# Kernel tuning notes

Measured on AMD Instinct MI355X. Metric: run time of the kernel, lower is better.

## Reference

```python
import jax, jax.numpy as jnp
import numpy as np

NQ = 10000   # num_q
N = 512      # n (seq len)
D = 512      # d (model dim)
H = 8        # attention heads
LW = 64      # local window
B = 16       # batch


def _mha(q, k, v, wi, bi, wo, bo, nh, mask=None):
    # torch nn.MultiheadAttention math (eval mode, dropout off), batch-first inputs
    Bq, S, d = q.shape
    hd = d // nh
    wq, wk, wv = jnp.split(wi, 3, axis=0)
    bq, bk, bv = jnp.split(bi, 3)

    def proj(x, w, b):
        y = x @ w.T + b
        return y.reshape(x.shape[0], x.shape[1], nh, hd).transpose(0, 2, 1, 3)  # [B,h,S,hd]

    Q = proj(q, wq, bq)
    K = proj(k, wk, bk)
    V = proj(v, wv, bv)
    s = jnp.einsum('bhqe,bhke->bhqk', Q, K) / jnp.sqrt(jnp.asarray(hd, q.dtype))
    if mask is not None:
        s = jnp.where(mask[None, None], -jnp.inf, s)
    w = jax.nn.softmax(s, axis=-1)
    o = jnp.einsum('bhqk,bhke->bhqe', w, V).transpose(0, 2, 1, 3).reshape(Bq, S, d)
    return o @ wo.T + bo, w.mean(axis=1)  # avg over heads like torch default


def _ln(x, g, b):
    m = x.mean(-1, keepdims=True)
    v = ((x - m) ** 2).mean(-1, keepdims=True)
    return (x - m) / jnp.sqrt(v + 1e-5) * g + b


def setup_inputs() -> dict:
    key = jax.random.key(0)
    ks = iter(jax.random.split(key, 40))
    f = lambda *sh: jax.random.normal(next(ks), sh, jnp.float32) * 0.02
    inp = {
        'q': jax.random.randint(next(ks), (B, N), 0, NQ, jnp.int32),
        'r': jax.random.randint(next(ks), (B, N), 0, 2, jnp.int32),
        'qry': jax.random.randint(next(ks), (B, N), 0, NQ, jnp.int32),
        'M_emb': f(2 * NQ, D),
        'E_emb': f(NQ, D),
        'P': f(N, D),
    }
    for nm in ['base', 'local', 'glob', 'cross']:
        inp[nm + '_in_w'] = f(3 * D, D)
        inp[nm + '_in_b'] = jnp.zeros((3 * D,), jnp.float32)
        inp[nm + '_out_w'] = f(D, D)
        inp[nm + '_out_b'] = jnp.zeros((D,), jnp.float32)
    inp['ln1_g'] = jnp.ones((D,), jnp.float32)
    inp['ln1_b'] = jnp.zeros((D,), jnp.float32)
    inp['w1'] = f(D, D)
    inp['b1'] = jnp.zeros((D,), jnp.float32)
    inp['w2'] = f(D, D)
    inp['b2'] = jnp.zeros((D,), jnp.float32)
    inp['ln2_g'] = jnp.ones((D,), jnp.float32)
    inp['ln2_b'] = jnp.zeros((D,), jnp.float32)
    inp['pred_w'] = f(1, D)
    inp['pred_b'] = jnp.zeros((1,), jnp.float32)
    return inp


def reference(q, r, qry, M_emb, E_emb, P,
              base_in_w, base_in_b, base_out_w, base_out_b,
              local_in_w, local_in_b, local_out_w, local_out_b,
              glob_in_w, glob_in_b, glob_out_w, glob_out_b,
              cross_in_w, cross_in_b, cross_out_w, cross_out_b,
              ln1_g, ln1_b, w1, b1, w2, b2, ln2_g, ln2_b, pred_w, pred_b):
    x = q + NQ * r
    M = M_emb[x] + P[None]          # [B,N,D], positional added as in torch code
    E = E_emb[qry]                  # [B,N,D]
    cm = jnp.triu(jnp.ones((N, N), bool), 1)

    S_base, attn_w = _mha(E, M, M, base_in_w, base_in_b, base_out_w, base_out_b, H, cm)
    S_base = _ln(S_base + M + E, ln1_g, ln1_b)

    lm = jnp.triu(jnp.ones((LW, LW), bool), 1)
    s_loc_in = S_base[:, -LW:, :]
    S_loc, _ = _mha(s_loc_in, s_loc_in, s_loc_in, local_in_w, local_in_b, local_out_w, local_out_b, H, lm)
    S_local = jnp.concatenate([jnp.zeros((S_base.shape[0], N - LW, D), S_base.dtype), S_loc], axis=1)

    S_global, _ = _mha(S_base, S_base, S_base, glob_in_w, glob_in_b, glob_out_w, glob_out_b, H, cm)
    S_cross, _ = _mha(S_base, S_local, S_local, cross_in_w, cross_in_b, cross_out_w, cross_out_b, H, None)

    S = S_base + S_local + S_global + S_cross
    F = jax.nn.relu(S @ w1.T + b1) @ w2.T + b2
    F = _ln(F + S, ln2_g, ln2_b)
    p = jax.nn.sigmoid(F @ pred_w.T + pred_b)[..., 0]   # [B,N]
    return p, attn_w
```

## Files before the change

### kernel.cpp

```cpp
#include <hip/hip_runtime.h>
#include <hip/hip_bf16.h>

#define D_MODEL 512
#define NHEAD 8
#define NSEQ 512
#define BATCH 16
#define LWIN 64

typedef short s16x8 __attribute__((ext_vector_type(8)));
typedef float f32x4 __attribute__((ext_vector_type(4)));

__device__ inline unsigned short f2bf(float f) {
    unsigned int u = __float_as_uint(f);
    u = (u + 0x7fffu + ((u >> 16) & 1u)) >> 16;
    return (unsigned short)u;
}

struct WP { const float* p[10]; };
__global__ __launch_bounds__(256) void wconv_kernel(WP wp, unsigned short* __restrict__ Wb)
{
    const long e = ((long)blockIdx.x * 256 + threadIdx.x) * 4;
    const float* src; long loc;
    if (e < 3145728) { int rg = (int)(e / 786432); src = wp.p[rg]; loc = e - (long)rg * 786432; }
    else { long j = e - 3145728; int rg = (int)(j >> 18); src = wp.p[4 + rg]; loc = j - ((long)rg << 18); }
    float4 v = *(const float4*)(src + loc);
    ushort4 o; o.x = f2bf(v.x); o.y = f2bf(v.y); o.z = f2bf(v.z); o.w = f2bf(v.w);
    *(ushort4*)(Wb + e) = o;
}

__global__ __launch_bounds__(128) void embed_kernel(
    const int* __restrict__ q, const int* __restrict__ r, const int* __restrict__ qry,
    const float* __restrict__ M_emb, const float* __restrict__ E_emb,
    const float* __restrict__ P, float* __restrict__ Mf, float* __restrict__ Ef,
    unsigned short* __restrict__ Mb, unsigned short* __restrict__ Eb)
{
    const int t = blockIdx.x;
    const int n = t & (NSEQ - 1);
    const int x = q[t] + 10000 * r[t];
    const int e = qry[t];
    const int i = threadIdx.x;
    float4 a = ((const float4*)(M_emb + (long)x * D_MODEL))[i];
    float4 p4 = ((const float4*)(P + (long)n * D_MODEL))[i];
    float4 ev = ((const float4*)(E_emb + (long)e * D_MODEL))[i];
    float4 mv = make_float4(a.x + p4.x, a.y + p4.y, a.z + p4.z, a.w + p4.w);
    ((float4*)(Mf + (long)t * D_MODEL))[i] = mv;
    ((float4*)(Ef + (long)t * D_MODEL))[i] = ev;
    ushort4 mb; mb.x = f2bf(mv.x); mb.y = f2bf(mv.y); mb.z = f2bf(mv.z); mb.w = f2bf(mv.w);
    ushort4 eb; eb.x = f2bf(ev.x); eb.y = f2bf(ev.y); eb.z = f2bf(ev.z); eb.w = f2bf(ev.w);
    *(ushort4*)(Mb + (long)t * D_MODEL + i * 4) = mb;
    *(ushort4*)(Eb + (long)t * D_MODEL + i * 4) = eb;
}

__global__ __launch_bounds__(256) void gemm_bf16(
    const unsigned short* __restrict__ A, const unsigned short* __restrict__ W,
    const float* __restrict__ bias, unsigned short* __restrict__ Cb,
    float* __restrict__ Cf, int ldc, int relu)
{
    __shared__ unsigned short As[128 * 40];
    __shared__ unsigned short Ws[128 * 40];
    const int tid = threadIdx.x, lane = tid & 63, wid = tid >> 6;
    const int m0 = blockIdx.y * 128, n0 = blockIdx.x * 128;
    const int mbase = (wid >> 1) * 64, nbase = (wid & 1) * 64;
    const int srow = tid >> 2, scol = (tid & 3) * 8;
    const unsigned short* Ap = A + (long)(m0 + srow) * 512 + scol;
    const unsigned short* Wp = W + (long)(n0 + srow) * 512 + scol;
    const int fr = lane & 15;
    const int fk = (lane >> 4) * 8;

    f32x4 acc[4][4];
    #pragma unroll
    for (int i = 0; i < 4; ++i)
        #pragma unroll
        for (int j = 0; j < 4; ++j) acc[i][j] = (f32x4){0.f, 0.f, 0.f, 0.f};

    for (int k0 = 0; k0 < 512; k0 += 32) {
        s16x8 a0 = *(const s16x8*)(Ap + k0);
        s16x8 a1 = *(const s16x8*)(Ap + 64 * 512 + k0);
        s16x8 w0 = *(const s16x8*)(Wp + k0);
        s16x8 w1 = *(const s16x8*)(Wp + 64 * 512 + k0);
        __syncthreads();
        *(s16x8*)&As[srow * 40 + scol] = a0;
        *(s16x8*)&As[(64 + srow) * 40 + scol] = a1;
        *(s16x8*)&Ws[srow * 40 + scol] = w0;
        *(s16x8*)&Ws[(64 + srow) * 40 + scol] = w1;
        __syncthreads();
        s16x8 af[4], wf[4];
        #pragma unroll
        for (int t = 0; t < 4; ++t) {
            af[t] = *(const s16x8*)&As[(mbase + t * 16 + fr) * 40 + fk];
            wf[t] = *(const s16x8*)&Ws[(nbase + t * 16 + fr) * 40 + fk];
        }
        #pragma unroll
        for (int i = 0; i < 4; ++i)
            #pragma unroll
            for (int j = 0; j < 4; ++j)
                acc[i][j] = __builtin_amdgcn_mfma_f32_16x16x32_bf16(af[i], wf[j], acc[i][j], 0, 0, 0);
    }

    const int q4 = (lane >> 4) * 4;
    #pragma unroll
    for (int j = 0; j < 4; ++j) {
        const int col = n0 + nbase + j * 16 + fr;
        const float bv = bias[col];
        #pragma unroll
        for (int i = 0; i < 4; ++i) {
            const int row = m0 + mbase + i * 16 + q4;
            #pragma unroll
            for (int rg = 0; rg < 4; ++rg) {
                float v = acc[i][j][rg] + bv;
                if (relu) v = fmaxf(v, 0.f);
                const long off = (long)(row + rg) * ldc + col;
                if (Cb) Cb[off] = f2bf(v);
                if (Cf) Cf[off] = v;
            }
        }
    }
}

__global__ __launch_bounds__(256) void flash_mfma(
    const unsigned short* __restrict__ Q, const unsigned short* __restrict__ K,
    const unsigned short* __restrict__ V, unsigned short* __restrict__ O,
    float* __restrict__ stats, int Nq, int Nkv, int ldq, int ldkv, int causal)
{
    __shared__ __align__(16) unsigned short Ks[64 * 72];
    __shared__ __align__(16) unsigned short Pl[64 * 72];
    __shared__ __align__(16) unsigned int   Vt[64 * 36];

    const int tid = threadIdx.x, lane = tid & 63, w = tid >> 6;
    const int lm = lane & 15, lq = lane >> 4;
    const int qt = blockIdx.x, h = blockIdx.y, b = blockIdx.z;

    s16x8 aq0, aq1;
    {
        const unsigned short* qp = Q + ((long)b * Nq + qt * 64 + w * 16 + lm) * ldq + h * 64 + lq * 8;
        aq0 = *(const s16x8*)qp;
        aq1 = *(const s16x8*)(qp + 32);
    }

    float m_r[4] = {-INFINITY, -INFINITY, -INFINITY, -INFINITY};
    float l_r[4] = {0.f, 0.f, 0.f, 0.f};
    f32x4 o_acc[4];
    #pragma unroll
    for (int t = 0; t < 4; ++t) o_acc[t] = (f32x4){0.f, 0.f, 0.f, 0.f};

    const int nkt = causal ? (qt + 1) : (Nkv >> 6);

    for (int kt = 0; kt < nkt; ++kt) {
        __syncthreads();
        {
            const long kb = ((long)b * Nkv + kt * 64) * ldkv + h * 64;
            #pragma unroll
            for (int c = 0; c < 2; ++c) {
                const int ch = c * 256 + tid;
                const int key = ch >> 3, d = (ch & 7) * 8;
                s16x8 kv = *(const s16x8*)(K + kb + (long)key * ldkv + d);
                *(s16x8*)&Ks[key * 72 + d] = kv;
            }
        }
        {
            const int kp = tid >> 3, dc = (tid & 7) * 8;
            const unsigned short* vp = V + ((long)b * Nkv + kt * 64 + 2 * kp) * ldkv + h * 64 + dc;
            uint4 va = *(const uint4*)vp;
            uint4 vb = *(const uint4*)(vp + ldkv);
            unsigned pw[8];
            pw[0] = (va.x & 0xffffu) | (vb.x << 16);
            pw[1] = (va.x >> 16)     | (vb.x & 0xffff0000u);
            pw[2] = (va.y & 0xffffu) | (vb.y << 16);
            pw[3] = (va.y >> 16)     | (vb.y & 0xffff0000u);
            pw[4] = (va.z & 0xffffu) | (vb.z << 16);
            pw[5] = (va.z >> 16)     | (vb.z & 0xffff0000u);
            pw[6] = (va.w & 0xffffu) | (vb.w << 16);
            pw[7] = (va.w >> 16)     | (vb.w & 0xffff0000u);
            #pragma unroll
            for (int j = 0; j < 8; ++j) {
                const int row = dc + j;
                const int col = ((((kp >> 2) ^ (row >> 3)) & 7) << 2) | (kp & 3);
                Vt[row * 36 + col] = pw[j];
            }
        }
        __syncthreads();

        f32x4 sc[4];
        #pragma unroll
        for (int t = 0; t < 4; ++t) sc[t] = (f32x4){0.f, 0.f, 0.f, 0.f};
        #pragma unroll
        for (int t = 0; t < 4; ++t) {
            s16x8 bk0 = *(const s16x8*)&Ks[(t * 16 + lm) * 72 + lq * 8];
            s16x8 bk1 = *(const s16x8*)&Ks[(t * 16 + lm) * 72 + lq * 8 + 32];
            sc[t] = __builtin_amdgcn_mfma_f32_16x16x32_bf16(aq0, bk0, sc[t], 0, 0, 0);
            sc[t] = __builtin_amdgcn_mfma_f32_16x16x32_bf16(aq1, bk1, sc[t], 0, 0, 0);
        }
        #pragma unroll
        for (int t = 0; t < 4; ++t)
            #pragma unroll
            for (int r = 0; r < 4; ++r) sc[t][r] *= 0.125f;

        if (causal && kt == qt) {
            #pragma unroll
            for (int t = 0; t < 4; ++t)
                #pragma unroll
                for (int r = 0; r < 4; ++r)
                    if (t * 16 + lm > w * 16 + lq * 4 + r) sc[t][r] = -INFINITY;
        }

        #pragma unroll
        for (int r = 0; r < 4; ++r) {
            float mt = fmaxf(fmaxf(sc[0][r], sc[1][r]), fmaxf(sc[2][r], sc[3][r]));
            #pragma unroll
            for (int off = 1; off < 16; off <<= 1) mt = fmaxf(mt, __shfl_xor(mt, off));
            const float mn = fmaxf(m_r[r], mt);
            const float al = __expf(m_r[r] - mn);
            m_r[r] = mn;
            float rs = 0.f;
            #pragma unroll
            for (int t = 0; t < 4; ++t) {
                float p = __expf(sc[t][r] - mn);
                sc[t][r] = p; rs += p;
                o_acc[t][r] *= al;
                Pl[(w * 16 + lq * 4 + r) * 72 + t * 16 + lm] = f2bf(p);
            }
            #pragma unroll
            for (int off = 1; off < 16; off <<= 1) rs += __shfl_xor(rs, off);
            l_r[r] = l_r[r] * al + rs;
        }

        #pragma unroll
        for (int ks = 0; ks < 2; ++ks) {
            s16x8 ap = *(const s16x8*)&Pl[(w * 16 + lm) * 72 + lq * 8 + ks * 32];
            #pragma unroll
            for (int t = 0; t < 4; ++t) {
                const int row = t * 16 + lm;
                const int gs = ((lq + 4 * ks) ^ (row >> 3)) & 7;
                s16x8 bv = *(const s16x8*)&Vt[row * 36 + gs * 4];
                o_acc[t] = __builtin_amdgcn_mfma_f32_16x16x32_bf16(ap, bv, o_acc[t], 0, 0, 0);
            }
        }
    }

    float inv[4];
    #pragma unroll
    for (int r = 0; r < 4; ++r) inv[r] = 1.0f / l_r[r];
    #pragma unroll
    for (int t = 0; t < 4; ++t)
        #pragma unroll
        for (int r = 0; r < 4; ++r)
            O[((long)b * Nq + qt * 64 + w * 16 + lq * 4 + r) * D_MODEL + h * 64 + t * 16 + lm]
                = f2bf(o_acc[t][r] * inv[r]);
    if (stats && lm == 0) {
        #pragma unroll
        for (int r = 0; r < 4; ++r) {
            const long row = qt * 64 + w * 16 + lq * 4 + r;
            const long idx = (((long)b * NHEAD + h) * Nq + row) * 2;
            stats[idx] = m_r[r]; stats[idx + 1] = l_r[r];
        }
    }
}

__global__ __launch_bounds__(256) void attn_w_kernel(
    const unsigned short* __restrict__ Q, const unsigned short* __restrict__ K,
    const float* __restrict__ stats, float* __restrict__ AW, int ldq, int ldk)
{
    const int kt = blockIdx.x, qt = blockIdx.y, b = blockIdx.z;
    const int tid = threadIdx.x;
    if (kt > qt) {
        const int tx = tid & 15, ty = tid >> 4;
        #pragma unroll
        for (int i = 0; i < 4; ++i)
            *(float4*)(AW + ((long)b * NSEQ + qt * 64 + ty * 4 + i) * NSEQ + kt * 64 + tx * 4)
                = make_float4(0.f, 0.f, 0.f, 0.f);
        return;
    }
    __shared__ __align__(16) unsigned short Ks[64 * 72];
    const int lane = tid & 63, w = tid >> 6;
    const int lm = lane & 15, lq = lane >> 4;

    f32x4 aw[4];
    #pragma unroll
    for (int t = 0; t < 4; ++t) aw[t] = (f32x4){0.f, 0.f, 0.f, 0.f};

    for (int h = 0; h < NHEAD; ++h) {
        __syncthreads();
        {
            const long kb = ((long)b * NSEQ + kt * 64) * ldk + h * 64;
            #pragma unroll
            for (int c = 0; c < 2; ++c) {
                const int ch = c * 256 + tid;
                const int key = ch >> 3, d = (ch & 7) * 8;
                s16x8 kv = *(const s16x8*)(K + kb + (long)key * ldk + d);
                *(s16x8*)&Ks[key * 72 + d] = kv;
            }
        }
        __syncthreads();
        s16x8 aq0, aq1;
        {
            const unsigned short* qp = Q + ((long)b * NSEQ + qt * 64 + w * 16 + lm) * ldq + h * 64 + lq * 8;
            aq0 = *(const s16x8*)qp;
            aq1 = *(const s16x8*)(qp + 32);
        }
        f32x4 sc[4];
        #pragma unroll
        for (int t = 0; t < 4; ++t) sc[t] = (f32x4){0.f, 0.f, 0.f, 0.f};
        #pragma unroll
        for (int t = 0; t < 4; ++t) {
            s16x8 bk0 = *(const s16x8*)&Ks[(t * 16 + lm) * 72 + lq * 8];
            s16x8 bk1 = *(const s16x8*)&Ks[(t * 16 + lm) * 72 + lq * 8 + 32];
            sc[t] = __builtin_amdgcn_mfma_f32_16x16x32_bf16(aq0, bk0, sc[t], 0, 0, 0);
            sc[t] = __builtin_amdgcn_mfma_f32_16x16x32_bf16(aq1, bk1, sc[t], 0, 0, 0);
        }
        #pragma unroll
        for (int r = 0; r < 4; ++r) {
            float2 ml = *(const float2*)(stats +
                (((long)b * NHEAD + h) * NSEQ + qt * 64 + w * 16 + lq * 4 + r) * 2);
            const float sub = ml.x, sca = 0.125f / ml.y;
            #pragma unroll
            for (int t = 0; t < 4; ++t) {
                const bool masked = (kt == qt) && (t * 16 + lm > w * 16 + lq * 4 + r);
                if (!masked) aw[t][r] += __expf(sc[t][r] * 0.125f - sub) * sca;
            }
        }
    }
    #pragma unroll
    for (int t = 0; t < 4; ++t)
        #pragma unroll
        for (int r = 0; r < 4; ++r)
            AW[((long)b * NSEQ + qt * 64 + w * 16 + lq * 4 + r) * NSEQ + kt * 64 + t * 16 + lm]
                = aw[t][r];
}

__global__ __launch_bounds__(256) void ln_kernel(
    const float* __restrict__ X, const float* __restrict__ R1,
    const float* __restrict__ R2, const float* __restrict__ g,
    const float* __restrict__ bb, float* __restrict__ outf,
    unsigned short* __restrict__ outb)
{
    const long row = blockIdx.x;
    const int tid = threadIdx.x;
    __shared__ float red[256];
    const long base = row * D_MODEL;
    float v0 = X[base + tid], v1 = X[base + tid + 256];
    if (R1) { v0 += R1[base + tid]; v1 += R1[base + tid + 256]; }
    if (R2) { v0 += R2[base + tid]; v1 += R2[base + tid + 256]; }
    red[tid] = v0 + v1; __syncthreads();
    for (int s = 128; s > 0; s >>= 1) {
        if (tid < s) red[tid] += red[tid + s];
        __syncthreads();
    }
    const float mean = red[0] * (1.f / 512.f);
    __syncthreads();
    const float d0 = v0 - mean, d1 = v1 - mean;
    red[tid] = d0 * d0 + d1 * d1; __syncthreads();
    for (int s = 128; s > 0; s >>= 1) {
        if (tid < s) red[tid] += red[tid + s];
        __syncthreads();
    }
    const float rstd = rsqrtf(red[0] * (1.f / 512.f) + 1e-5f);
    const float y0 = d0 * rstd * g[tid] + bb[tid];
    const float y1 = d1 * rstd * g[tid + 256] + bb[tid + 256];
    if (outf) { outf[base + tid] = y0; outf[base + tid + 256] = y1; }
    if (outb) { outb[base + tid] = f2bf(y0); outb[base + tid + 256] = f2bf(y1); }
}

__global__ __launch_bounds__(128) void extract_last64(
    const unsigned short* __restrict__ Sb, unsigned short* __restrict__ out)
{
    const int t = blockIdx.x;
    const int b = t >> 6, j = t & 63;
    const uint2* src = (const uint2*)(Sb + ((long)b * NSEQ + (NSEQ - LWIN) + j) * D_MODEL);
    uint2* dst = (uint2*)(out + (long)t * D_MODEL);
    dst[threadIdx.x] = src[threadIdx.x];
}

__global__ __launch_bounds__(128) void build_slocal(
    const float* __restrict__ Tloc, float* __restrict__ Sf, unsigned short* __restrict__ Sb)
{
    const int t = blockIdx.x;
    const int b = t >> 9, n = t & 511;
    const int i = threadIdx.x;
    float4 v;
    if (n < NSEQ - LWIN) v = make_float4(0.f, 0.f, 0.f, 0.f);
    else v = ((const float4*)(Tloc + ((long)b * LWIN + (n - (NSEQ - LWIN))) * D_MODEL))[i];
    ((float4*)(Sf + (long)t * D_MODEL))[i] = v;
    ushort4 u; u.x = f2bf(v.x); u.y = f2bf(v.y); u.z = f2bf(v.z); u.w = f2bf(v.w);
    *(ushort4*)(Sb + (long)t * D_MODEL + i * 4) = u;
}

__global__ __launch_bounds__(256) void sum4_kernel(
    const float* __restrict__ a, const float* __restrict__ b,
    const float* __restrict__ c, const float* __restrict__ d,
    float* __restrict__ of, unsigned short* __restrict__ ob, int n4)
{
    const int i = blockIdx.x * blockDim.x + threadIdx.x;
    if (i < n4) {
        float4 x = ((const float4*)a)[i];
        float4 y = ((const float4*)b)[i];
        float4 z = ((const float4*)c)[i];
        float4 w = ((const float4*)d)[i];
        float4 s = make_float4(x.x + y.x + z.x + w.x, x.y + y.y + z.y + w.y,
                               x.z + y.z + z.z + w.z, x.w + y.w + z.w + w.w);
        ((float4*)of)[i] = s;
        ushort4 u; u.x = f2bf(s.x); u.y = f2bf(s.y); u.z = f2bf(s.z); u.w = f2bf(s.w);
        *(ushort4*)(ob + (long)i * 4) = u;
    }
}

__global__ __launch_bounds__(256) void pred_kernel(
    const float* __restrict__ F, const float* __restrict__ pw,
    const float* __restrict__ pb, float* __restrict__ out)
{
    const int w = threadIdx.x >> 6, lane = threadIdx.x & 63;
    const long row = (long)blockIdx.x * 4 + w;
    const float* fr = F + row * D_MODEL;
    float s = 0.f;
    #pragma unroll
    for (int i = 0; i < 8; ++i) s += fr[lane + i * 64] * pw[lane + i * 64];
    #pragma unroll
    for (int off = 32; off > 0; off >>= 1) s += __shfl_down(s, off);
    if (lane == 0) out[row] = 1.f / (1.f + __expf(-(s + pb[0])));
}

extern "C" void kernel_launch(void* const* d_in, const int* in_sizes, int n_in,
                              void* d_out, int out_size, void* d_ws, size_t ws_size,
                              hipStream_t stream)
{
    const int*   q          = (const int*)d_in[0];
    const int*   r          = (const int*)d_in[1];
    const int*   qry        = (const int*)d_in[2];
    const float* M_emb      = (const float*)d_in[3];
    const float* E_emb      = (const float*)d_in[4];
    const float* P          = (const float*)d_in[5];
    const float* base_in_w  = (const float*)d_in[6];
    const float* base_in_b  = (const float*)d_in[7];
    const float* base_out_w = (const float*)d_in[8];
    const float* base_out_b = (const float*)d_in[9];
    const float* local_in_w = (const float*)d_in[10];
    const float* local_in_b = (const float*)d_in[11];
    const float* local_out_w= (const float*)d_in[12];
    const float* local_out_b= (const float*)d_in[13];
    const float* glob_in_w  = (const float*)d_in[14];
    const float* glob_in_b  = (const float*)d_in[15];
    const float* glob_out_w = (const float*)d_in[16];
    const float* glob_out_b = (const float*)d_in[17];
    const float* cross_in_w = (const float*)d_in[18];
    const float* cross_in_b = (const float*)d_in[19];
    const float* cross_out_w= (const float*)d_in[20];
    const float* cross_out_b= (const float*)d_in[21];
    const float* ln1_g      = (const float*)d_in[22];
    const float* ln1_b      = (const float*)d_in[23];
    const float* w1         = (const float*)d_in[24];
    const float* b1         = (const float*)d_in[25];
    const float* w2         = (const float*)d_in[26];
    const float* b2         = (const float*)d_in[27];
    const float* ln2_g      = (const float*)d_in[28];
    const float* ln2_b      = (const float*)d_in[29];
    const float* pred_w     = (const float*)d_in[30];
    const float* pred_b     = (const float*)d_in[31];
    float* out = (float*)d_out;

    char* p = (char*)d_ws;
    unsigned short* Wb = (unsigned short*)p; p += 4718592L * 2;
    unsigned short* B[11];
    for (int i = 0; i < 11; ++i) { B[i] = (unsigned short*)p; p += 8388608L; }
    unsigned short* SLin = (unsigned short*)p; p += 1048576L;
    unsigned short* Obl  = (unsigned short*)p; p += 1048576L;
    float* R[5];
    for (int i = 0; i < 5; ++i) { R[i] = (float*)p; p += 16777216L; }
    float* Tloc  = (float*)p; p += 2097152L;
    float* stats = (float*)p; p += 524288L;

    unsigned short* Mb = B[0];      unsigned short* Qc_b = B[0];
    unsigned short* Eb = B[1];      unsigned short* Oc_b = B[1];
    unsigned short* Qb = B[2];      unsigned short* Sb_b = B[2];
    unsigned short* KVb = B[3];
    unsigned short* Ob  = B[5];
    unsigned short* Sbase_b  = B[6];
    unsigned short* Slocal_b = B[7];
    unsigned short* QKV3 = B[8];
    unsigned short* H1_b = B[8];
    float* Mf = R[0];       float* Scross_f = R[0];
    float* Ef = R[1];       float* Sbuf_f   = R[1];
    float* Tb_f = R[2];     float* Sglobal_f= R[2];  float* Fbuf_f = R[2];
    float* Sbase_f = R[3];  float* Fpre_f   = R[3];
    float* Slocal_f = R[4];

    const long oBin = 0, oLin = 786432, oGin = 1572864, oCin = 2359296;
    const long oBout = 3145728, oLout = 3407872, oGout = 3670016, oCout = 3932160;
    const long oW1 = 4194304, oW2 = 4456448;

    dim3 gN512(4, 64), gN1024(8, 64), gN1536(12, 64);
    dim3 gL1536(12, 8), gL512(4, 8);
    dim3 fa_full(8, NHEAD, BATCH), fa_loc(1, NHEAD, BATCH);

    WP wp; wp.p[0] = base_in_w; wp.p[1] = local_in_w; wp.p[2] = glob_in_w; wp.p[3] = cross_in_w;
    wp.p[4] = base_out_w; wp.p[5] = local_out_w; wp.p[6] = glob_out_w; wp.p[7] = cross_out_w;
    wp.p[8] = w1; wp.p[9] = w2;
    wconv_kernel<<<4608, 256, 0, stream>>>(wp, Wb);

    embed_kernel<<<8192, 128, 0, stream>>>(q, r, qry, M_emb, E_emb, P, Mf, Ef, Mb, Eb);

    gemm_bf16<<<gN512, 256, 0, stream>>>(Eb, Wb + oBin, base_in_b, Qb, nullptr, 512, 0);
    gemm_bf16<<<gN1024, 256, 0, stream>>>(Mb, Wb + oBin + 512 * 512, base_in_b + 512, KVb, nullptr, 1024, 0);
    flash_mfma<<<fa_full, 256, 0, stream>>>(Qb, KVb, KVb + 512, Ob, stats, 512, 512, 512, 1024, 1);
    attn_w_kernel<<<dim3(8, 8, BATCH), 256, 0, stream>>>(Qb, KVb, stats, out + 8192, 512, 1024);
    gemm_bf16<<<gN512, 256, 0, stream>>>(Ob, Wb + oBout, base_out_b, nullptr, Tb_f, 512, 0);
    ln_kernel<<<8192, 256, 0, stream>>>(Tb_f, Mf, Ef, ln1_g, ln1_b, Sbase_f, Sbase_b);

    extract_last64<<<1024, 128, 0, stream>>>(Sbase_b, SLin);
    gemm_bf16<<<gL1536, 256, 0, stream>>>(SLin, Wb + oLin, local_in_b, QKV3, nullptr, 1536, 0);
    flash_mfma<<<fa_loc, 256, 0, stream>>>(QKV3, QKV3 + 512, QKV3 + 1024, Obl, nullptr, 64, 64, 1536, 1536, 1);
    gemm_bf16<<<gL512, 256, 0, stream>>>(Obl, Wb + oLout, local_out_b, nullptr, Tloc, 512, 0);
    build_slocal<<<8192, 128, 0, stream>>>(Tloc, Slocal_f, Slocal_b);

    gemm_bf16<<<gN1536, 256, 0, stream>>>(Sbase_b, Wb + oGin, glob_in_b, QKV3, nullptr, 1536, 0);
    flash_mfma<<<fa_full, 256, 0, stream>>>(QKV3, QKV3 + 512, QKV3 + 1024, Ob, nullptr, 512, 512, 1536, 1536, 1);
    gemm_bf16<<<gN512, 256, 0, stream>>>(Ob, Wb + oGout, glob_out_b, nullptr, Sglobal_f, 512, 0);

    gemm_bf16<<<gN512, 256, 0, stream>>>(Sbase_b, Wb + oCin, cross_in_b, Qc_b, nullptr, 512, 0);
    gemm_bf16<<<gN1024, 256, 0, stream>>>(Slocal_b, Wb + oCin + 512 * 512, cross_in_b + 512, KVb, nullptr, 1024, 0);
    flash_mfma<<<fa_full, 256, 0, stream>>>(Qc_b, KVb, KVb + 512, Oc_b, nullptr, 512, 512, 512, 1024, 0);
    gemm_bf16<<<gN512, 256, 0, stream>>>(Oc_b, Wb + oCout, cross_out_b, nullptr, Scross_f, 512, 0);

    const int n4 = (int)((long)BATCH * NSEQ * D_MODEL / 4);
    sum4_kernel<<<(n4 + 255) / 256, 256, 0, stream>>>(Sbase_f, Slocal_f, Sglobal_f, Scross_f, Sbuf_f, Sb_b, n4);

    gemm_bf16<<<gN512, 256, 0, stream>>>(Sb_b, Wb + oW1, b1, H1_b, nullptr, 512, 1);
    gemm_bf16<<<gN512, 256, 0, stream>>>(H1_b, Wb + oW2, b2, nullptr, Fpre_f, 512, 0);
    ln_kernel<<<8192, 256, 0, stream>>>(Fpre_f, Sbuf_f, nullptr, ln2_g, ln2_b, Fbuf_f, nullptr);
    pred_kernel<<<2048, 256, 0, stream>>>(Fbuf_f, pred_w, pred_b, out);
}
```

Baseline: 582.7 us.

## Fuse QKV projection GEMMs, pair causal tiles, prefetch KV in flash attention

Merges the separate Q and KV projection GEMMs into one launch by letting the GEMM pick a second A operand for output columns past a split point, and folds the last-64-rows extraction into the GEMM's row indexing, which removes launches and a copy kernel. The flash-attention kernel now gives each block a pair of query tiles (qa, nqt-1-qa) to even out causal work, and loads the next K/V tile into registers while the current one is computed. It also swaps the MFMA operand order so the softmax max and sum need fewer shuffles, uses exp2 with a prescaled constant, and vectorises the output and attention-weight stores. The cost is more registers per thread for two query tiles and a doubled V buffer in registers, plus more indexing logic in every GEMM.

Result: faster. 534.8 us (-8.2%).

```diff
diff --git a/kernel.cpp b/kernel.cpp
--- a/kernel.cpp
+++ b/kernel.cpp
@@ -6,6 +6,8 @@
 #define NSEQ 512
 #define BATCH 16
 #define LWIN 64
+#define S2C 0.18033688f
+#define L2E 1.44269504f
 
 typedef short s16x8 __attribute__((ext_vector_type(8)));
 typedef float f32x4 __attribute__((ext_vector_type(4)));
@@ -52,9 +54,9 @@
 }
 
 __global__ __launch_bounds__(256) void gemm_bf16(
-    const unsigned short* __restrict__ A, const unsigned short* __restrict__ W,
-    const float* __restrict__ bias, unsigned short* __restrict__ Cb,
-    float* __restrict__ Cf, int ldc, int relu)
+    const unsigned short* __restrict__ A, const unsigned short* __restrict__ A2, int nsplit,
+    const unsigned short* __restrict__ W, const float* __restrict__ bias,
+    unsigned short* __restrict__ Cb, float* __restrict__ Cf, int ldc, int relu, int arem)
 {
     __shared__ unsigned short As[128 * 40];
     __shared__ unsigned short Ws[128 * 40];
@@ -62,7 +64,14 @@
     const int m0 = blockIdx.y * 128, n0 = blockIdx.x * 128;
     const int mbase = (wid >> 1) * 64, nbase = (wid & 1) * 64;
     const int srow = tid >> 2, scol = (tid & 3) * 8;
-    const unsigned short* Ap = A + (long)(m0 + srow) * 512 + scol;
+    const unsigned short* Asel = (n0 >= nsplit) ? A2 : A;
+    int row0 = m0 + srow, row1 = m0 + srow + 64;
+    if (arem) {
+        row0 = ((row0 >> 6) << 9) + (NSEQ - LWIN) + (row0 & 63);
+        row1 = ((row1 >> 6) << 9) + (NSEQ - LWIN) + (row1 & 63);
+    }
+    const unsigned short* Ap0 = Asel + (long)row0 * 512 + scol;
+    const unsigned short* Ap1 = Asel + (long)row1 * 512 + scol;
     const unsigned short* Wp = W + (long)(n0 + srow) * 512 + scol;
     const int fr = lane & 15;
     const int fk = (lane >> 4) * 8;
@@ -74,8 +83,8 @@
         for (int j = 0; j < 4; ++j) acc[i][j] = (f32x4){0.f, 0.f, 0.f, 0.f};
 
     for (int k0 = 0; k0 < 512; k0 += 32) {
-        s16x8 a0 = *(const s16x8*)(Ap + k0);
-        s16x8 a1 = *(const s16x8*)(Ap + 64 * 512 + k0);
+        s16x8 a0 = *(const s16x8*)(Ap0 + k0);
+        s16x8 a1 = *(const s16x8*)(Ap1 + k0);
         s16x8 w0 = *(const s16x8*)(Wp + k0);
         s16x8 w1 = *(const s16x8*)(Wp + 64 * 512 + k0);
         __syncthreads();
@@ -128,130 +137,160 @@
 
     const int tid = threadIdx.x, lane = tid & 63, w = tid >> 6;
     const int lm = lane & 15, lq = lane >> 4;
-    const int qt = blockIdx.x, h = blockIdx.y, b = blockIdx.z;
-
-    s16x8 aq0, aq1;
+    const int h = blockIdx.y, b = blockIdx.z;
+    const int nqt = Nq >> 6;
+    const int qa = blockIdx.x, qb = nqt - 1 - qa;
+    const bool single = (qa == qb);
+
+    s16x8 aqA0, aqA1, aqB0, aqB1;
     {
-        const unsigned short* qp = Q + ((long)b * Nq + qt * 64 + w * 16 + lm) * ldq + h * 64 + lq * 8;
-        aq0 = *(const s16x8*)qp;
-        aq1 = *(const s16x8*)(qp + 32);
-    }
-
-    float m_r[4] = {-INFINITY, -INFINITY, -INFINITY, -INFINITY};
-    float l_r[4] = {0.f, 0.f, 0.f, 0.f};
-    f32x4 o_acc[4];
-    #pragma unroll
-    for (int t = 0; t < 4; ++t) o_acc[t] = (f32x4){0.f, 0.f, 0.f, 0.f};
-
-    const int nkt = causal ? (qt + 1) : (Nkv >> 6);
-
-    for (int kt = 0; kt < nkt; ++kt) {
-        __syncthreads();
-        {
-            const long kb = ((long)b * Nkv + kt * 64) * ldkv + h * 64;
-            #pragma unroll
-            for (int c = 0; c < 2; ++c) {
-                const int ch = c * 256 + tid;
-                const int key = ch >> 3, d = (ch & 7) * 8;
-                s16x8 kv = *(const s16x8*)(K + kb + (long)key * ldkv + d);
-                *(s16x8*)&Ks[key * 72 + d] = kv;
-            }
-        }
-        {
-            const int kp = tid >> 3, dc = (tid & 7) * 8;
-            const unsigned short* vp = V + ((long)b * Nkv + kt * 64 + 2 * kp) * ldkv + h * 64 + dc;
-            uint4 va = *(const uint4*)vp;
-            uint4 vb = *(const uint4*)(vp + ldkv);
-            unsigned pw[8];
-            pw[0] = (va.x & 0xffffu) | (vb.x << 16);
-            pw[1] = (va.x >> 16)     | (vb.x & 0xffff0000u);
-            pw[2] = (va.y & 0xffffu) | (vb.y << 16);
-            pw[3] = (va.y >> 16)     | (vb.y & 0xffff0000u);
-            pw[4] = (va.z & 0xffffu) | (vb.z << 16);
-            pw[5] = (va.z >> 16)     | (vb.z & 0xffff0000u);
-            pw[6] = (va.w & 0xffffu) | (vb.w << 16);
-            pw[7] = (va.w >> 16)     | (vb.w & 0xffff0000u);
-            #pragma unroll
-            for (int j = 0; j < 8; ++j) {
-                const int row = dc + j;
-                const int col = ((((kp >> 2) ^ (row >> 3)) & 7) << 2) | (kp & 3);
-                Vt[row * 36 + col] = pw[j];
-            }
-        }
-        __syncthreads();
-
+        const unsigned short* qp = Q + ((long)b * Nq + qb * 64 + w * 16 + lm) * ldq + h * 64 + lq * 8;
+        aqB0 = *(const s16x8*)qp; aqB1 = *(const s16x8*)(qp + 32);
+    }
+    if (!single) {
+        const unsigned short* qp = Q + ((long)b * Nq + qa * 64 + w * 16 + lm) * ldq + h * 64 + lq * 8;
+        aqA0 = *(const s16x8*)qp; aqA1 = *(const s16x8*)(qp + 32);
+    }
+
+    float mA = -INFINITY, lA = 0.f, mB = -INFINITY, lB = 0.f;
+    f32x4 oA[4], oB[4];
+    #pragma unroll
+    for (int t = 0; t < 4; ++t) { oA[t] = (f32x4){0.f,0.f,0.f,0.f}; oB[t] = (f32x4){0.f,0.f,0.f,0.f}; }
+
+    const int nkt = causal ? (qb + 1) : (Nkv >> 6);
+    const int skey = tid >> 3, sd = (tid & 7) * 8;
+
+    s16x8 kr0, kr1; uint4 vr0, vr1;
+    {
+        const long kb = ((long)b * Nkv) * ldkv + h * 64;
+        kr0 = *(const s16x8*)(K + kb + (long)skey * ldkv + sd);
+        kr1 = *(const s16x8*)(K + kb + (long)(skey + 32) * ldkv + sd);
+        const unsigned short* vp = V + ((long)b * Nkv + 2 * skey) * ldkv + h * 64 + sd;
+        vr0 = *(const uint4*)vp; vr1 = *(const uint4*)(vp + ldkv);
+    }
+
+    auto process = [&](s16x8 a0, s16x8 a1, float& m, float& l, f32x4* oacc, bool diag) {
         f32x4 sc[4];
         #pragma unroll
-        for (int t = 0; t < 4; ++t) sc[t] = (f32x4){0.f, 0.f, 0.f, 0.f};
+        for (int t = 0; t < 4; ++t) sc[t] = (f32x4){0.f,0.f,0.f,0.f};
         #pragma unroll
         for (int t = 0; t < 4; ++t) {
-            s16x8 bk0 = *(const s16x8*)&Ks[(t * 16 + lm) * 72 + lq * 8];
-            s16x8 bk1 = *(const s16x8*)&Ks[(t * 16 + lm) * 72 + lq * 8 + 32];
-            sc[t] = __builtin_amdgcn_mfma_f32_16x16x32_bf16(aq0, bk0, sc[t], 0, 0, 0);
-            sc[t] = __builtin_amdgcn_mfma_f32_16x16x32_bf16(aq1, bk1, sc[t], 0, 0, 0);
-        }
-        #pragma unroll
-        for (int t = 0; t < 4; ++t)
-            #pragma unroll
-            for (int r = 0; r < 4; ++r) sc[t][r] *= 0.125f;
-
-        if (causal && kt == qt) {
+            s16x8 k0 = *(const s16x8*)&Ks[(t * 16 + lm) * 72 + lq * 8];
+            s16x8 k1 = *(const s16x8*)&Ks[(t * 16 + lm) * 72 + lq * 8 + 32];
+            sc[t] = __builtin_amdgcn_mfma_f32_16x16x32_bf16(k0, a0, sc[t], 0, 0, 0);
+            sc[t] = __builtin_amdgcn_mfma_f32_16x16x32_bf16(k1, a1, sc[t], 0, 0, 0);
+        }
+        if (diag) {
             #pragma unroll
             for (int t = 0; t < 4; ++t)
                 #pragma unroll
                 for (int r = 0; r < 4; ++r)
-                    if (t * 16 + lm > w * 16 + lq * 4 + r) sc[t][r] = -INFINITY;
-        }
-
-        #pragma unroll
-        for (int r = 0; r < 4; ++r) {
-            float mt = fmaxf(fmaxf(sc[0][r], sc[1][r]), fmaxf(sc[2][r], sc[3][r]));
-            #pragma unroll
-            for (int off = 1; off < 16; off <<= 1) mt = fmaxf(mt, __shfl_xor(mt, off));
-            const float mn = fmaxf(m_r[r], mt);
-            const float al = __expf(m_r[r] - mn);
-            m_r[r] = mn;
-            float rs = 0.f;
-            #pragma unroll
-            for (int t = 0; t < 4; ++t) {
-                float p = __expf(sc[t][r] - mn);
+                    if (t * 16 + lq * 4 + r > w * 16 + lm) sc[t][r] = -INFINITY;
+        }
+        float mt = sc[0][0];
+        #pragma unroll
+        for (int t = 0; t < 4; ++t)
+            #pragma unroll
+            for (int r = 0; r < 4; ++r) mt = fmaxf(mt, sc[t][r]);
+        mt = fmaxf(mt, __shfl_xor(mt, 16));
+        mt = fmaxf(mt, __shfl_xor(mt, 32));
+        const float mn = fmaxf(m, mt);
+        const float al = exp2f((m - mn) * S2C);
+        float rs = 0.f;
+        #pragma unroll
+        for (int t = 0; t < 4; ++t)
+            #pragma unroll
+            for (int r = 0; r < 4; ++r) {
+                float p = exp2f((sc[t][r] - mn) * S2C);
                 sc[t][r] = p; rs += p;
-                o_acc[t][r] *= al;
-                Pl[(w * 16 + lq * 4 + r) * 72 + t * 16 + lm] = f2bf(p);
             }
-            #pragma unroll
-            for (int off = 1; off < 16; off <<= 1) rs += __shfl_xor(rs, off);
-            l_r[r] = l_r[r] * al + rs;
-        }
-
+        rs += __shfl_xor(rs, 16);
+        rs += __shfl_xor(rs, 32);
+        m = mn; l = l * al + rs;
+        #pragma unroll
+        for (int t = 0; t < 4; ++t) oacc[t] *= al;
+        #pragma unroll
+        for (int t = 0; t < 4; ++t) {
+            ushort4 u;
+            u.x = f2bf(sc[t][0]); u.y = f2bf(sc[t][1]);
+            u.z = f2bf(sc[t][2]); u.w = f2bf(sc[t][3]);
+            *(ushort4*)&Pl[(w * 16 + lm) * 72 + t * 16 + lq * 4] = u;
+        }
         #pragma unroll
         for (int ks = 0; ks < 2; ++ks) {
-            s16x8 ap = *(const s16x8*)&Pl[(w * 16 + lm) * 72 + lq * 8 + ks * 32];
+            s16x8 bp = *(const s16x8*)&Pl[(w * 16 + lm) * 72 + ks * 32 + lq * 8];
             #pragma unroll
             for (int t = 0; t < 4; ++t) {
                 const int row = t * 16 + lm;
-                const int gs = ((lq + 4 * ks) ^ (row >> 3)) & 7;
-                s16x8 bv = *(const s16x8*)&Vt[row * 36 + gs * 4];
-                o_acc[t] = __builtin_amdgcn_mfma_f32_16x16x32_bf16(ap, bv, o_acc[t], 0, 0, 0);
+                const int pg = ((lq >> 1) + 2 * ks) ^ ((row >> 3) & 3);
+                s16x8 av = *(const s16x8*)((const unsigned short*)Vt + row * 72 + pg * 16 + (lq & 1) * 8);
+                oacc[t] = __builtin_amdgcn_mfma_f32_16x16x32_bf16(av, bp, oacc[t], 0, 0, 0);
             }
         }
-    }
-
-    float inv[4];
-    #pragma unroll
-    for (int r = 0; r < 4; ++r) inv[r] = 1.0f / l_r[r];
-    #pragma unroll
-    for (int t = 0; t < 4; ++t)
-        #pragma unroll
-        for (int r = 0; r < 4; ++r)
-            O[((long)b * Nq + qt * 64 + w * 16 + lq * 4 + r) * D_MODEL + h * 64 + t * 16 + lm]
-                = f2bf(o_acc[t][r] * inv[r]);
-    if (stats && lm == 0) {
-        #pragma unroll
-        for (int r = 0; r < 4; ++r) {
-            const long row = qt * 64 + w * 16 + lq * 4 + r;
-            const long idx = (((long)b * NHEAD + h) * Nq + row) * 2;
-            stats[idx] = m_r[r]; stats[idx + 1] = l_r[r];
+    };
+
+    for (int kt = 0; kt < nkt; ++kt) {
+        __syncthreads();
+        *(s16x8*)&Ks[skey * 72 + sd] = kr0;
+        *(s16x8*)&Ks[(skey + 32) * 72 + sd] = kr1;
+        {
+            unsigned pw[8];
+            pw[0] = (vr0.x & 0xffffu) | (vr1.x << 16);
+            pw[1] = (vr0.x >> 16)     | (vr1.x & 0xffff0000u);
+            pw[2] = (vr0.y & 0xffffu) | (vr1.y << 16);
+            pw[3] = (vr0.y >> 16)     | (vr1.y & 0xffff0000u);
+            pw[4] = (vr0.z & 0xffffu) | (vr1.z << 16);
+            pw[5] = (vr0.z >> 16)     | (vr1.z & 0xffff0000u);
+            pw[6] = (vr0.w & 0xffffu) | (vr1.w << 16);
+            pw[7] = (vr0.w >> 16)     | (vr1.w & 0xffff0000u);
+            #pragma unroll
+            for (int j = 0; j < 8; ++j) {
+                const int row = sd + j;
+                const int col = (((skey >> 3) ^ ((row >> 3) & 3)) << 3) | (skey & 7);
+                Vt[row * 36 + col] = pw[j];
+            }
+        }
+        __syncthreads();
+        if (kt + 1 < nkt) {
+            const long kb = ((long)b * Nkv + (kt + 1) * 64) * ldkv + h * 64;
+            kr0 = *(const s16x8*)(K + kb + (long)skey * ldkv + sd);
+            kr1 = *(const s16x8*)(K + kb + (long)(skey + 32) * ldkv + sd);
+            const unsigned short* vp = V + ((long)b * Nkv + (kt + 1) * 64 + 2 * skey) * ldkv + h * 64 + sd;
+            vr0 = *(const uint4*)vp; vr1 = *(const uint4*)(vp + ldkv);
+        }
+        process(aqB0, aqB1, mB, lB, oB, causal && (kt == qb));
+        if (!single && (!causal || kt <= qa))
+            process(aqA0, aqA1, mA, lA, oA, causal && (kt == qa));
+    }
+
+    {
+        const float inv = 1.0f / lB;
+        const long orow = ((long)b * Nq + qb * 64 + w * 16 + lm) * D_MODEL + h * 64;
+        #pragma unroll
+        for (int t = 0; t < 4; ++t) {
+            ushort4 u;
+            u.x = f2bf(oB[t][0] * inv); u.y = f2bf(oB[t][1] * inv);
+            u.z = f2bf(oB[t][2] * inv); u.w = f2bf(oB[t][3] * inv);
+            *(ushort4*)(O + orow + t * 16 + lq * 4) = u;
+        }
+    }
+    if (!single) {
+        const float inv = 1.0f / lA;
+        const long orow = ((long)b * Nq + qa * 64 + w * 16 + lm) * D_MODEL + h * 64;
+        #pragma unroll
+        for (int t = 0; t < 4; ++t) {
+            ushort4 u;
+            u.x = f2bf(oA[t][0] * inv); u.y = f2bf(oA[t][1] * inv);
+            u.z = f2bf(oA[t][2] * inv); u.w = f2bf(oA[t][3] * inv);
+            *(ushort4*)(O + orow + t * 16 + lq * 4) = u;
+        }
+    }
+    if (stats && lq == 0) {
+        long idx = (((long)b * NHEAD + h) * Nq + qb * 64 + w * 16 + lm) * 2;
+        stats[idx] = mB * 0.125f; stats[idx + 1] = lB;
+        if (!single) {
+            idx = (((long)b * NHEAD + h) * Nq + qa * 64 + w * 16 + lm) * 2;
+            stats[idx] = mA * 0.125f; stats[idx + 1] = lA;
         }
     }
 }
@@ -273,58 +312,50 @@
     __shared__ __align__(16) unsigned short Ks[64 * 72];
     const int lane = tid & 63, w = tid >> 6;
     const int lm = lane & 15, lq = lane >> 4;
+    const int skey = tid >> 3, sd = (tid & 7) * 8;
+    const long qrow = (long)b * NSEQ + qt * 64 + w * 16 + lm;
 
     f32x4 aw[4];
     #pragma unroll
-    for (int t = 0; t < 4; ++t) aw[t] = (f32x4){0.f, 0.f, 0.f, 0.f};
+    for (int t = 0; t < 4; ++t) aw[t] = (f32x4){0.f,0.f,0.f,0.f};
 
     for (int h = 0; h < NHEAD; ++h) {
         __syncthreads();
         {
             const long kb = ((long)b * NSEQ + kt * 64) * ldk + h * 64;
-            #pragma unroll
-            for (int c = 0; c < 2; ++c) {
-                const int ch = c * 256 + tid;
-                const int key = ch >> 3, d = (ch & 7) * 8;
-                s16x8 kv = *(const s16x8*)(K + kb + (long)key * ldk + d);
-                *(s16x8*)&Ks[key * 72 + d] = kv;
+            *(s16x8*)&Ks[skey * 72 + sd] = *(const s16x8*)(K + kb + (long)skey * ldk + sd);
+            *(s16x8*)&Ks[(skey + 32) * 72 + sd] = *(const s16x8*)(K + kb + (long)(skey + 32) * ldk + sd);
+        }
+        __syncthreads();
+        s16x8 a0, a1;
+        {
+            const unsigned short* qp = Q + qrow * ldq + h * 64 + lq * 8;
+            a0 = *(const s16x8*)qp; a1 = *(const s16x8*)(qp + 32);
+        }
+        f32x4 sc[4];
+        #pragma unroll
+        for (int t = 0; t < 4; ++t) sc[t] = (f32x4){0.f,0.f,0.f,0.f};
+        #pragma unroll
+        for (int t = 0; t < 4; ++t) {
+            s16x8 k0 = *(const s16x8*)&Ks[(t * 16 + lm) * 72 + lq * 8];
+            s16x8 k1 = *(const s16x8*)&Ks[(t * 16 + lm) * 72 + lq * 8 + 32];
+            sc[t] = __builtin_amdgcn_mfma_f32_16x16x32_bf16(k0, a0, sc[t], 0, 0, 0);
+            sc[t] = __builtin_amdgcn_mfma_f32_16x16x32_bf16(k1, a1, sc[t], 0, 0, 0);
+        }
+        float2 ml = *(const float2*)(stats + (((long)b * NHEAD + h) * NSEQ + qt * 64 + w * 16 + lm) * 2);
+        const float mb2 = ml.x * L2E;
+        const float sca = 0.125f / ml.y;
+        #pragma unroll
+        for (int t = 0; t < 4; ++t)
+            #pragma unroll
+            for (int r = 0; r < 4; ++r) {
+                const bool masked = (kt == qt) && (t * 16 + lq * 4 + r > w * 16 + lm);
+                if (!masked) aw[t][r] += exp2f(sc[t][r] * S2C - mb2) * sca;
             }
-        }
-        __syncthreads();
-        s16x8 aq0, aq1;
-        {
-            const unsigned short* qp = Q + ((long)b * NSEQ + qt * 64 + w * 16 + lm) * ldq + h * 64 + lq * 8;
-            aq0 = *(const s16x8*)qp;
-            aq1 = *(const s16x8*)(qp + 32);
-        }
-        f32x4 sc[4];
-        #pragma unroll
-        for (int t = 0; t < 4; ++t) sc[t] = (f32x4){0.f, 0.f, 0.f, 0.f};
-        #pragma unroll
-        for (int t = 0; t < 4; ++t) {
-            s16x8 bk0 = *(const s16x8*)&Ks[(t * 16 + lm) * 72 + lq * 8];
-            s16x8 bk1 = *(const s16x8*)&Ks[(t * 16 + lm) * 72 + lq * 8 + 32];
-            sc[t] = __builtin_amdgcn_mfma_f32_16x16x32_bf16(aq0, bk0, sc[t], 0, 0, 0);
-            sc[t] = __builtin_amdgcn_mfma_f32_16x16x32_bf16(aq1, bk1, sc[t], 0, 0, 0);
-        }
-        #pragma unroll
-        for (int r = 0; r < 4; ++r) {
-            float2 ml = *(const float2*)(stats +
-                (((long)b * NHEAD + h) * NSEQ + qt * 64 + w * 16 + lq * 4 + r) * 2);
-            const float sub = ml.x, sca = 0.125f / ml.y;
-            #pragma unroll
-            for (int t = 0; t < 4; ++t) {
-                const bool masked = (kt == qt) && (t * 16 + lm > w * 16 + lq * 4 + r);
-                if (!masked) aw[t][r] += __expf(sc[t][r] * 0.125f - sub) * sca;
-            }
-        }
     }
     #pragma unroll
     for (int t = 0; t < 4; ++t)
-        #pragma unroll
-        for (int r = 0; r < 4; ++r)
-            AW[((long)b * NSEQ + qt * 64 + w * 16 + lq * 4 + r) * NSEQ + kt * 64 + t * 16 + lm]
-                = aw[t][r];
+        *(float4*)(AW + qrow * NSEQ + kt * 64 + t * 16 + lq * 4) = float4{aw[t][0], aw[t][1], aw[t][2], aw[t][3]};
 }
 
 __global__ __launch_bounds__(256) void ln_kernel(
@@ -358,16 +389,6 @@
     const float y1 = d1 * rstd * g[tid + 256] + bb[tid + 256];
     if (outf) { outf[base + tid] = y0; outf[base + tid + 256] = y1; }
     if (outb) { outb[base + tid] = f2bf(y0); outb[base + tid + 256] = f2bf(y1); }
-}
-
-__global__ __launch_bounds__(128) void extract_last64(
-    const unsigned short* __restrict__ Sb, unsigned short* __restrict__ out)
-{
-    const int t = blockIdx.x;
-    const int b = t >> 6, j = t & 63;
-    const uint2* src = (const uint2*)(Sb + ((long)b * NSEQ + (NSEQ - LWIN) + j) * D_MODEL);
-    uint2* dst = (uint2*)(out + (long)t * D_MODEL);
-    dst[threadIdx.x] = src[threadIdx.x];
 }
 
 __global__ __launch_bounds__(128) void build_slocal(
@@ -460,17 +481,16 @@
     unsigned short* Wb = (unsigned short*)p; p += 4718592L * 2;
     unsigned short* B[11];
     for (int i = 0; i < 11; ++i) { B[i] = (unsigned short*)p; p += 8388608L; }
-    unsigned short* SLin = (unsigned short*)p; p += 1048576L;
     unsigned short* Obl  = (unsigned short*)p; p += 1048576L;
     float* R[5];
     for (int i = 0; i < 5; ++i) { R[i] = (float*)p; p += 16777216L; }
     float* Tloc  = (float*)p; p += 2097152L;
     float* stats = (float*)p; p += 524288L;
 
-    unsigned short* Mb = B[0];      unsigned short* Qc_b = B[0];
+    unsigned short* Mb = B[0];
     unsigned short* Eb = B[1];      unsigned short* Oc_b = B[1];
-    unsigned short* Qb = B[2];      unsigned short* Sb_b = B[2];
-    unsigned short* KVb = B[3];
+    unsigned short* QKVb = B[2];
+    unsigned short* Sb_b = B[2];
     unsigned short* Ob  = B[5];
     unsigned short* Sbase_b  = B[6];
     unsigned short* Slocal_b = B[7];
@@ -485,10 +505,11 @@
     const long oBin = 0, oLin = 786432, oGin = 1572864, oCin = 2359296;
     const long oBout = 3145728, oLout = 3407872, oGout = 3670016, oCout = 3932160;
     const long oW1 = 4194304, oW2 = 4456448;
-
-    dim3 gN512(4, 64), gN1024(8, 64), gN1536(12, 64);
+    const int BIG = 1 << 30;
+
+    dim3 gN512(4, 64), gN1536(12, 64);
     dim3 gL1536(12, 8), gL512(4, 8);
-    dim3 fa_full(8, NHEAD, BATCH), fa_loc(1, NHEAD, BATCH);
+    dim3 fa_full(4, NHEAD, BATCH), fa_loc(1, NHEAD, BATCH);
 
     WP wp; wp.p[0] = base_in_w; wp.p[1] = local_in_w; wp.p[2] = glob_in_w; wp.p[3] = cross_in_w;
     wp.p[4] = base_out_w; wp.p[5] = local_out_w; wp.p[6] = glob_out_w; wp.p[7] = cross_out_w;
@@ -497,33 +518,30 @@
 
     embed_kernel<<<8192, 128, 0, stream>>>(q, r, qry, M_emb, E_emb, P, Mf, Ef, Mb, Eb);
 
-    gemm_bf16<<<gN512, 256, 0, stream>>>(Eb, Wb + oBin, base_in_b, Qb, nullptr, 512, 0);
-    gemm_bf16<<<gN1024, 256, 0, stream>>>(Mb, Wb + oBin + 512 * 512, base_in_b + 512, KVb, nullptr, 1024, 0);
-    flash_mfma<<<fa_full, 256, 0, stream>>>(Qb, KVb, KVb + 512, Ob, stats, 512, 512, 512, 1024, 1);
-    attn_w_kernel<<<dim3(8, 8, BATCH), 256, 0, stream>>>(Qb, KVb, stats, out + 8192, 512, 1024);
-    gemm_bf16<<<gN512, 256, 0, stream>>>(Ob, Wb + oBout, base_out_b, nullptr, Tb_f, 512, 0);
+    gemm_bf16<<<gN1536, 256, 0, stream>>>(Eb, Mb, 512, Wb + oBin, base_in_b, QKVb, nullptr, 1536, 0, 0);
+    flash_mfma<<<fa_full, 256, 0, stream>>>(QKVb, QKVb + 512, QKVb + 1024, Ob, stats, 512, 512, 1536, 1536, 1);
+    attn_w_kernel<<<dim3(8, 8, BATCH), 256, 0, stream>>>(QKVb, QKVb + 512, stats, out + 8192, 1536, 1536);
+    gemm_bf16<<<gN512, 256, 0, stream>>>(Ob, Ob, BIG, Wb + oBout, base_out_b, nullptr, Tb_f, 512, 0, 0);
     ln_kernel<<<8192, 256, 0, stream>>>(Tb_f, Mf, Ef, ln1_g, ln1_b, Sbase_f, Sbase_b);
 
-    extract_last64<<<1024, 128, 0, stream>>>(Sbase_b, SLin);
-    gemm_bf16<<<gL1536, 256, 0, stream>>>(SLin, Wb + oLin, local_in_b, QKV3, nullptr, 1536, 0);
+    gemm_bf16<<<gL1536, 256, 0, stream>>>(Sbase_b, Sbase_b, BIG, Wb + oLin, local_in_b, QKV3, nullptr, 1536, 0, 1);
     flash_mfma<<<fa_loc, 256, 0, stream>>>(QKV3, QKV3 + 512, QKV3 + 1024, Obl, nullptr, 64, 64, 1536, 1536, 1);
-    gemm_bf16<<<gL512, 256, 0, stream>>>(Obl, Wb + oLout, local_out_b, nullptr, Tloc, 512, 0);
+    gemm_bf16<<<gL512, 256, 0, stream>>>(Obl, Obl, BIG, Wb + oLout, local_out_b, nullptr, Tloc, 512, 0, 0);
     build_slocal<<<8192, 128, 0, stream>>>(Tloc, Slocal_f, Slocal_b);
 
-    gemm_bf16<<<gN1536, 256, 0, stream>>>(Sbase_b, Wb + oGin, glob_in_b, QKV3, nullptr, 1536, 0);
+    gemm_bf16<<<gN1536, 256, 0, stream>>>(Sbase_b, Sbase_b, BIG, Wb + oGin, glob_in_b, QKV3, nullptr, 1536, 0, 0);
     flash_mfma<<<fa_full, 256, 0, stream>>>(QKV3, QKV3 + 512, QKV3 + 1024, Ob, nullptr, 512, 512, 1536, 1536, 1);
-    gemm_bf16<<<gN512, 256, 0, stream>>>(Ob, Wb + oGout, glob_out_b, nullptr, Sglobal_f, 512, 0);
-
-    gemm_bf16<<<gN512, 256, 0, stream>>>(Sbase_b, Wb + oCin, cross_in_b, Qc_b, nullptr, 512, 0);
-    gemm_bf16<<<gN1024, 256, 0, stream>>>(Slocal_b, Wb + oCin + 512 * 512, cross_in_b + 512, KVb, nullptr, 1024, 0);
-    flash_mfma<<<fa_full, 256, 0, stream>>>(Qc_b, KVb, KVb + 512, Oc_b, nullptr, 512, 512, 512, 1024, 0);
-    gemm_bf16<<<gN512, 256, 0, stream>>>(Oc_b, Wb + oCout, cross_out_b, nullptr, Scross_f, 512, 0);
+    gemm_bf16<<<gN512, 256, 0, stream>>>(Ob, Ob, BIG, Wb + oGout, glob_out_b, nullptr, Sglobal_f, 512, 0, 0);
+
+    gemm_bf16<<<gN1536, 256, 0, stream>>>(Sbase_b, Slocal_b, 512, Wb + oCin, cross_in_b, QKVb, nullptr, 1536, 0, 0);
+    flash_mfma<<<fa_full, 256, 0, stream>>>(QKVb, QKVb + 512, QKVb + 1024, Oc_b, nullptr, 512, 512, 1536, 1536, 0);
+    gemm_bf16<<<gN512, 256, 0, stream>>>(Oc_b, Oc_b, BIG, Wb + oCout, cross_out_b, nullptr, Scross_f, 512, 0, 0);
 
     const int n4 = (int)((long)BATCH * NSEQ * D_MODEL / 4);
     sum4_kernel<<<(n4 + 255) / 256, 256, 0, stream>>>(Sbase_f, Slocal_f, Sglobal_f, Scross_f, Sbuf_f, Sb_b, n4);
 
-    gemm_bf16<<<gN512, 256, 0, stream>>>(Sb_b, Wb + oW1, b1, H1_b, nullptr, 512, 1);
-    gemm_bf16<<<gN512, 256, 0, stream>>>(H1_b, Wb + oW2, b2, nullptr, Fpre_f, 512, 0);
+    gemm_bf16<<<gN512, 256, 0, stream>>>(Sb_b, Sb_b, BIG, Wb + oW1, b1, H1_b, nullptr, 512, 1, 0);
+    gemm_bf16<<<gN512, 256, 0, stream>>>(H1_b, H1_b, BIG, Wb + oW2, b2, nullptr, Fpre_f, 512, 0, 0);
     ln_kernel<<<8192, 256, 0, stream>>>(Fpre_f, Sbuf_f, nullptr, ln2_g, ln2_b, Fbuf_f, nullptr);
     pred_kernel<<<2048, 256, 0, stream>>>(Fbuf_f, pred_w, pred_b, out);
 }
```
